# Kernel optimization log

Measured on AMD Instinct MI355X. Metric: run time of the kernel, lower is better.

The kernel has to match this reference:

```python
import jax, jax.numpy as jnp
import numpy as np

CELU_ALPHA = 3.0  # hardcoded in the torch module (nn.CELU(alpha=3.0), F.celu(alpha=3.0))

def celu(x):
    # celu(x, a) = max(0, x) + min(0, a*(exp(x/a)-1)); overflow-safe form
    return jnp.maximum(x, 0.0) + CELU_ALPHA * jnp.expm1(jnp.minimum(x, 0.0) / CELU_ALPHA)

def setup_inputs() -> dict:
    key = jax.random.key(0)
    k1, k2, k3, k4, k5 = jax.random.split(key, 5)
    N, E, H, D = 16384, 262144, 4, 64
    return {
        "features": jax.random.normal(k1, (N, D), dtype=jnp.float32),
        "metapath_embedding": jax.random.normal(k2, (E, D), dtype=jnp.float32),
        "attn1_w": jax.random.normal(k3, (H, D), dtype=jnp.float32) * 0.15,  # xavier-ish scale
        "attn2": jax.random.normal(k4, (H, D), dtype=jnp.float32) * 0.15,
        "segment_ids": jax.random.randint(k5, (E,), 0, N, dtype=jnp.int32),
    }

def reference(features, metapath_embedding, attn1_w, attn2, segment_ids):
    N, D = features.shape
    H = attn1_w.shape[0]
    # eft: same embedding broadcast over heads (torch.cat([emb]*H).view(-1,H,D))
    eft = celu(metapath_embedding)                    # [E, D]
    a1 = celu(features @ attn1_w.T)                   # [N, H] (per-node, shared across its instances)
    a2 = eft @ attn2.T                                # [E, H]
    a = celu(a1[segment_ids] + a2)                    # [E, H]
    # segment softmax over instances of each node
    m = jax.lax.stop_gradient(jax.ops.segment_max(a, segment_ids, num_segments=N))  # [N, H]
    ex = jnp.exp(a - m[segment_ids])                  # [E, H]
    denom = jax.ops.segment_sum(ex, segment_ids, num_segments=N)                    # [N, H]
    att = ex / denom[segment_ids]                     # [E, H]
    # weighted sum of eft over each node's instances -> [N, H, D]
    msg = jax.ops.segment_sum(att[:, :, None] * eft[:, None, :], segment_ids, num_segments=N)
    # empty segments yield 0 and celu(0)=0, matching the torch zero-fill branch
    return celu(msg).reshape(N, H * D)
```

## Files before the change

### kernel.cpp

```cpp
#include <hip/hip_runtime.h>
#include <math.h>

#define CAP 64

__device__ __forceinline__ float celu3(float x) {
    return fmaxf(x, 0.0f) + 3.0f * (__expf(fminf(x, 0.0f) * (1.0f / 3.0f)) - 1.0f);
}

__device__ __forceinline__ float wave_sum64(float v) {
#pragma unroll
    for (int off = 32; off > 0; off >>= 1) v += __shfl_xor(v, off, 64);
    return v;
}


__global__ __launch_bounds__(256) void zero_kernel(int* __restrict__ p, int n) {
    int i = blockIdx.x * 256 + threadIdx.x;
    if (i < n) p[i] = 0;
}


__global__ __launch_bounds__(256) void hist_a1_kernel(
    const int* __restrict__ seg, int* __restrict__ counts, int* __restrict__ elist, int E,
    const float* __restrict__ feat, const float* __restrict__ w1,
    float* __restrict__ a1, int N)
{
    int nblk_a1 = (N + 3) / 4;
    if ((int)blockIdx.x < nblk_a1) {
        int lane = threadIdx.x & 63;
        int wv = threadIdx.x >> 6;
        int n = blockIdx.x * 4 + wv;
        if (n >= N) return;
        float f = feat[(long)n * 64 + lane];
        float s[4];
#pragma unroll
        for (int h = 0; h < 4; ++h) s[h] = wave_sum64(f * w1[h * 64 + lane]);
        if (lane < 4) a1[n * 4 + lane] = celu3(s[lane]);
    } else {
        int i = (blockIdx.x - nblk_a1) * blockDim.x + threadIdx.x;
        int stride = 512 * blockDim.x;
        for (; i < E; i += stride) {
            int s = seg[i];
            int r = atomicAdd(&counts[s], 1);
            if (r < CAP) elist[s * CAP + r] = i;
        }
    }
}


__global__ __launch_bounds__(256) void fused_kernel(
    const float* __restrict__ meta, const float* __restrict__ w2,
    const float* __restrict__ a1, const int* __restrict__ counts,
    const int* __restrict__ elist, const int* __restrict__ seg,
    float* __restrict__ out, int N, int E)
{
    int t = threadIdx.x;
    int lane = t & 63;
    int wv = t >> 6;
    int n = blockIdx.x * 4 + wv;
    if (n >= N) return;

    int cnt = counts[n];
    int g = lane >> 4;
    int q = lane & 15;
    long ob = (long)n * 256 + g * 64 + q * 4;

    if (cnt == 0) {
        float4 z = {0.f, 0.f, 0.f, 0.f};
        *(float4*)(out + ob) = z;
        return;
    }

    float4 a1v = *(const float4*)(a1 + (long)n * 4);

    if (cnt <= CAP) {
        float4 w2q0 = *(const float4*)(w2 + 0 * 64 + q * 4);
        float4 w2q1 = *(const float4*)(w2 + 1 * 64 + q * 4);
        float4 w2q2 = *(const float4*)(w2 + 2 * 64 + q * 4);
        float4 w2q3 = *(const float4*)(w2 + 3 * 64 + q * 4);

        int eid_l = (lane < cnt) ? elist[n * CAP + lane] : 0;

        float sp0 = 0.f, sp1 = 0.f, sp2 = 0.f, sp3 = 0.f;
        float4 acc0 = {0,0,0,0}, acc1 = {0,0,0,0}, acc2 = {0,0,0,0}, acc3 = {0,0,0,0};

        int nch = (cnt + 3) >> 2;
#pragma unroll 4
        for (int c = 0; c < nch; ++c) {
            int j = c * 4 + g;
            bool vr = j < cnt;
            int eid = __shfl(eid_l, j);
            float4 v = *(const float4*)(meta + (long)eid * 64 + q * 4);
            float4 ef;
            ef.x = celu3(v.x); ef.y = celu3(v.y); ef.z = celu3(v.z); ef.w = celu3(v.w);

            float d0 = ef.x * w2q0.x + ef.y * w2q0.y + ef.z * w2q0.z + ef.w * w2q0.w;
            float d1 = ef.x * w2q1.x + ef.y * w2q1.y + ef.z * w2q1.z + ef.w * w2q1.w;
            float d2 = ef.x * w2q2.x + ef.y * w2q2.y + ef.z * w2q2.z + ef.w * w2q2.w;
            float d3 = ef.x * w2q3.x + ef.y * w2q3.y + ef.z * w2q3.z + ef.w * w2q3.w;
#pragma unroll
            for (int off = 1; off < 16; off <<= 1) {
                d0 += __shfl_xor(d0, off); d1 += __shfl_xor(d1, off);
                d2 += __shfl_xor(d2, off); d3 += __shfl_xor(d3, off);
            }

            float A0 = vr ? celu3(a1v.x + d0) : -INFINITY;
            float A1 = vr ? celu3(a1v.y + d1) : -INFINITY;
            float A2 = vr ? celu3(a1v.z + d2) : -INFINITY;
            float A3 = vr ? celu3(a1v.w + d3) : -INFINITY;

            float p0 = __expf(fminf(A0, 80.f));
            float p1 = __expf(fminf(A1, 80.f));
            float p2 = __expf(fminf(A2, 80.f));
            float p3 = __expf(fminf(A3, 80.f));

            sp0 += p0; sp1 += p1; sp2 += p2; sp3 += p3;

            acc0.x = fmaf(p0, ef.x, acc0.x); acc0.y = fmaf(p0, ef.y, acc0.y);
            acc0.z = fmaf(p0, ef.z, acc0.z); acc0.w = fmaf(p0, ef.w, acc0.w);
            acc1.x = fmaf(p1, ef.x, acc1.x); acc1.y = fmaf(p1, ef.y, acc1.y);
            acc1.z = fmaf(p1, ef.z, acc1.z); acc1.w = fmaf(p1, ef.w, acc1.w);
            acc2.x = fmaf(p2, ef.x, acc2.x); acc2.y = fmaf(p2, ef.y, acc2.y);
            acc2.z = fmaf(p2, ef.z, acc2.z); acc2.w = fmaf(p2, ef.w, acc2.w);
            acc3.x = fmaf(p3, ef.x, acc3.x); acc3.y = fmaf(p3, ef.y, acc3.y);
            acc3.z = fmaf(p3, ef.z, acc3.z); acc3.w = fmaf(p3, ef.w, acc3.w);
        }

        sp0 += __shfl_xor(sp0, 16); sp0 += __shfl_xor(sp0, 32);
        sp1 += __shfl_xor(sp1, 16); sp1 += __shfl_xor(sp1, 32);
        sp2 += __shfl_xor(sp2, 16); sp2 += __shfl_xor(sp2, 32);
        sp3 += __shfl_xor(sp3, 16); sp3 += __shfl_xor(sp3, 32);

        acc0.x += __shfl_xor(acc0.x, 16); acc0.x += __shfl_xor(acc0.x, 32);
        acc0.y += __shfl_xor(acc0.y, 16); acc0.y += __shfl_xor(acc0.y, 32);
        acc0.z += __shfl_xor(acc0.z, 16); acc0.z += __shfl_xor(acc0.z, 32);
        acc0.w += __shfl_xor(acc0.w, 16); acc0.w += __shfl_xor(acc0.w, 32);
        acc1.x += __shfl_xor(acc1.x, 16); acc1.x += __shfl_xor(acc1.x, 32);
        acc1.y += __shfl_xor(acc1.y, 16); acc1.y += __shfl_xor(acc1.y, 32);
        acc1.z += __shfl_xor(acc1.z, 16); acc1.z += __shfl_xor(acc1.z, 32);
        acc1.w += __shfl_xor(acc1.w, 16); acc1.w += __shfl_xor(acc1.w, 32);
        acc2.x += __shfl_xor(acc2.x, 16); acc2.x += __shfl_xor(acc2.x, 32);
        acc2.y += __shfl_xor(acc2.y, 16); acc2.y += __shfl_xor(acc2.y, 32);
        acc2.z += __shfl_xor(acc2.z, 16); acc2.z += __shfl_xor(acc2.z, 32);
        acc2.w += __shfl_xor(acc2.w, 16); acc2.w += __shfl_xor(acc2.w, 32);
        acc3.x += __shfl_xor(acc3.x, 16); acc3.x += __shfl_xor(acc3.x, 32);
        acc3.y += __shfl_xor(acc3.y, 16); acc3.y += __shfl_xor(acc3.y, 32);
        acc3.z += __shfl_xor(acc3.z, 16); acc3.z += __shfl_xor(acc3.z, 32);
        acc3.w += __shfl_xor(acc3.w, 16); acc3.w += __shfl_xor(acc3.w, 32);

        float rs0 = 1.f / sp0, rs1 = 1.f / sp1, rs2 = 1.f / sp2, rs3 = 1.f / sp3;

        float4 av = (g == 0) ? acc0 : (g == 1) ? acc1 : (g == 2) ? acc2 : acc3;
        float rg = (g == 0) ? rs0 : (g == 1) ? rs1 : (g == 2) ? rs2 : rs3;
        float4 o;
        o.x = celu3(av.x * rg); o.y = celu3(av.y * rg);
        o.z = celu3(av.z * rg); o.w = celu3(av.w * rg);
        *(float4*)(out + ob) = o;
        return;
    }

    {
        float a10 = a1v.x, a11 = a1v.y, a12 = a1v.z, a13 = a1v.w;
        float w2v0 = w2[0 * 64 + lane], w2v1 = w2[1 * 64 + lane];
        float w2v2 = w2[2 * 64 + lane], w2v3 = w2[3 * 64 + lane];
        float m0 = -INFINITY, m1 = -INFINITY, m2 = -INFINITY, m3 = -INFINITY;
        float s0 = 0.f, s1 = 0.f, s2 = 0.f, s3 = 0.f;
        float ac0 = 0.f, ac1 = 0.f, ac2 = 0.f, ac3 = 0.f;
        for (int base = 0; base < E; base += 64) {
            int e = base + lane;
            bool hit = (e < E) && (seg[e] == n);
            unsigned long long ball = __ballot(hit);
            while (ball) {
                int b = __ffsll((long long)ball) - 1;
                ball &= ball - 1;
                int eid = base + b;
                float eft = celu3(meta[(long)eid * 64 + lane]);
                float d0 = wave_sum64(eft * w2v0);
                float d1 = wave_sum64(eft * w2v1);
                float d2 = wave_sum64(eft * w2v2);
                float d3 = wave_sum64(eft * w2v3);
                float A0 = celu3(a10 + d0), A1 = celu3(a11 + d1);
                float A2 = celu3(a12 + d2), A3 = celu3(a13 + d3);
                float nm0 = fmaxf(m0, A0), nm1 = fmaxf(m1, A1);
                float nm2 = fmaxf(m2, A2), nm3 = fmaxf(m3, A3);
                float al0 = __expf(m0 - nm0), al1 = __expf(m1 - nm1);
                float al2 = __expf(m2 - nm2), al3 = __expf(m3 - nm3);
                float p0 = __expf(A0 - nm0), p1 = __expf(A1 - nm1);
                float p2 = __expf(A2 - nm2), p3 = __expf(A3 - nm3);
                s0 = fmaf(al0, s0, p0); s1 = fmaf(al1, s1, p1);
                s2 = fmaf(al2, s2, p2); s3 = fmaf(al3, s3, p3);
                ac0 = fmaf(p0, eft, al0 * ac0); ac1 = fmaf(p1, eft, al1 * ac1);
                ac2 = fmaf(p2, eft, al2 * ac2); ac3 = fmaf(p3, eft, al3 * ac3);
                m0 = nm0; m1 = nm1; m2 = nm2; m3 = nm3;
            }
        }
        long ob2 = (long)n * 256 + lane;
        out[ob2]       = celu3(ac0 / s0);
        out[ob2 + 64]  = celu3(ac1 / s1);
        out[ob2 + 128] = celu3(ac2 / s2);
        out[ob2 + 192] = celu3(ac3 / s3);
    }
}


extern "C" void kernel_launch(void* const* d_in, const int* in_sizes, int n_in,
                              void* d_out, int out_size, void* d_ws, size_t ws_size,
                              hipStream_t stream)
{
    const float* feat = (const float*)d_in[0];
    const float* meta = (const float*)d_in[1];
    const float* w1   = (const float*)d_in[2];
    const float* w2   = (const float*)d_in[3];
    const int*   seg  = (const int*)d_in[4];
    float* out = (float*)d_out;

    int N = in_sizes[0] / 64;
    int E = in_sizes[4];

    float* a1   = (float*)d_ws;
    int* counts = (int*)(a1 + (size_t)N * 4);
    int* elist  = counts + N;

    int nblk_a1 = (N + 3) / 4;

    zero_kernel<<<(N + 255) / 256, 256, 0, stream>>>(counts, N);
    hist_a1_kernel<<<nblk_a1 + 512, 256, 0, stream>>>(seg, counts, elist, E, feat, w1, a1, N);
    fused_kernel<<<(N + 3) / 4, 256, 0, stream>>>(meta, w2, a1, counts, elist, seg, out, N, E);
}
```

Measured before the change: 55.17 us.

## Precompute per-edge attention dot products in a separate pass before node aggregation

Moves the per-edge celu(meta)·attn2 dot product out of the per-node gather loop into a streaming pass, one thread per edge. That pass runs in the same launch as the histogram atomics and writes a float4 per edge to workspace. The node kernel then computes softmax weights once per edge in-lane and broadcasts them with shuffles, dropping the 16-lane shuffle reductions. The zeroing kernel is folded into the a1 kernel to save a launch. The trade-off is a second full read of the metapath embeddings plus extra workspace traffic for the dot products.

Measured after the change: 58.39 us. 1.06x slower.

```diff
diff --git a/kernel.cpp b/kernel.cpp
--- a/kernel.cpp
+++ b/kernel.cpp
@@ -14,45 +14,71 @@
 }
 
 
-__global__ __launch_bounds__(256) void zero_kernel(int* __restrict__ p, int n) {
-    int i = blockIdx.x * 256 + threadIdx.x;
-    if (i < n) p[i] = 0;
-}
-
-
-__global__ __launch_bounds__(256) void hist_a1_kernel(
+__global__ __launch_bounds__(256) void init_kernel(
+    int* __restrict__ counts, int N,
+    const float* __restrict__ feat, const float* __restrict__ w1,
+    float* __restrict__ a1)
+{
+    int nblk_zero = (N + 255) / 256;
+    if ((int)blockIdx.x < nblk_zero) {
+        int i = blockIdx.x * 256 + threadIdx.x;
+        if (i < N) counts[i] = 0;
+        return;
+    }
+    int n = (blockIdx.x - nblk_zero) * 4 + (threadIdx.x >> 6);
+    int lane = threadIdx.x & 63;
+    if (n >= N) return;
+    float f = feat[(long)n * 64 + lane];
+    float s[4];
+#pragma unroll
+    for (int h = 0; h < 4; ++h) s[h] = wave_sum64(f * w1[h * 64 + lane]);
+    if (lane < 4) a1[n * 4 + lane] = celu3(s[lane]);
+}
+
+
+__global__ __launch_bounds__(256) void hist_dot_kernel(
     const int* __restrict__ seg, int* __restrict__ counts, int* __restrict__ elist, int E,
-    const float* __restrict__ feat, const float* __restrict__ w1,
-    float* __restrict__ a1, int N)
-{
-    int nblk_a1 = (N + 3) / 4;
-    if ((int)blockIdx.x < nblk_a1) {
-        int lane = threadIdx.x & 63;
-        int wv = threadIdx.x >> 6;
-        int n = blockIdx.x * 4 + wv;
-        if (n >= N) return;
-        float f = feat[(long)n * 64 + lane];
-        float s[4];
-#pragma unroll
-        for (int h = 0; h < 4; ++h) s[h] = wave_sum64(f * w1[h * 64 + lane]);
-        if (lane < 4) a1[n * 4 + lane] = celu3(s[lane]);
-    } else {
-        int i = (blockIdx.x - nblk_a1) * blockDim.x + threadIdx.x;
-        int stride = 512 * blockDim.x;
+    const float* __restrict__ meta, const float* __restrict__ w2,
+    float4* __restrict__ d4)
+{
+    if ((int)blockIdx.x < 512) {
+        int i = blockIdx.x * 256 + threadIdx.x;
+        int stride = 512 * 256;
         for (; i < E; i += stride) {
             int s = seg[i];
             int r = atomicAdd(&counts[s], 1);
             if (r < CAP) elist[s * CAP + r] = i;
         }
-    }
-}
-
-
-__global__ __launch_bounds__(256) void fused_kernel(
+        return;
+    }
+    int e = (blockIdx.x - 512) * 256 + threadIdx.x;
+    if (e >= E) return;
+    const float4* row = (const float4*)(meta + (long)e * 64);
+    float d0 = 0.f, d1 = 0.f, d2 = 0.f, d3 = 0.f;
+#pragma unroll
+    for (int k = 0; k < 16; ++k) {
+        float4 v = row[k];
+        float4 ef;
+        ef.x = celu3(v.x); ef.y = celu3(v.y); ef.z = celu3(v.z); ef.w = celu3(v.w);
+        float4 w0 = *(const float4*)(w2 + 0 * 64 + k * 4);
+        float4 w1v = *(const float4*)(w2 + 1 * 64 + k * 4);
+        float4 w2v = *(const float4*)(w2 + 2 * 64 + k * 4);
+        float4 w3v = *(const float4*)(w2 + 3 * 64 + k * 4);
+        d0 += ef.x * w0.x + ef.y * w0.y + ef.z * w0.z + ef.w * w0.w;
+        d1 += ef.x * w1v.x + ef.y * w1v.y + ef.z * w1v.z + ef.w * w1v.w;
+        d2 += ef.x * w2v.x + ef.y * w2v.y + ef.z * w2v.z + ef.w * w2v.w;
+        d3 += ef.x * w3v.x + ef.y * w3v.y + ef.z * w3v.z + ef.w * w3v.w;
+    }
+    float4 o; o.x = d0; o.y = d1; o.z = d2; o.w = d3;
+    d4[e] = o;
+}
+
+
+__global__ __launch_bounds__(256) void node_kernel(
     const float* __restrict__ meta, const float* __restrict__ w2,
     const float* __restrict__ a1, const int* __restrict__ counts,
-    const int* __restrict__ elist, const int* __restrict__ seg,
-    float* __restrict__ out, int N, int E)
+    const int* __restrict__ elist, const float4* __restrict__ d4,
+    const int* __restrict__ seg, float* __restrict__ out, int N, int E)
 {
     int t = threadIdx.x;
     int lane = t & 63;
@@ -74,56 +100,44 @@
     float4 a1v = *(const float4*)(a1 + (long)n * 4);
 
     if (cnt <= CAP) {
-        float4 w2q0 = *(const float4*)(w2 + 0 * 64 + q * 4);
-        float4 w2q1 = *(const float4*)(w2 + 1 * 64 + q * 4);
-        float4 w2q2 = *(const float4*)(w2 + 2 * 64 + q * 4);
-        float4 w2q3 = *(const float4*)(w2 + 3 * 64 + q * 4);
-
-        int eid_l = (lane < cnt) ? elist[n * CAP + lane] : 0;
+        bool valid = lane < cnt;
+        int eid_l = valid ? elist[n * CAP + lane] : 0;
+        float p0 = 0.f, p1 = 0.f, p2 = 0.f, p3 = 0.f;
+        if (valid) {
+            float4 dv = d4[eid_l];
+            float A0 = celu3(a1v.x + dv.x);
+            float A1 = celu3(a1v.y + dv.y);
+            float A2 = celu3(a1v.z + dv.z);
+            float A3 = celu3(a1v.w + dv.w);
+            p0 = __expf(fminf(A0, 80.f));
+            p1 = __expf(fminf(A1, 80.f));
+            p2 = __expf(fminf(A2, 80.f));
+            p3 = __expf(fminf(A3, 80.f));
+        }
 
         float sp0 = 0.f, sp1 = 0.f, sp2 = 0.f, sp3 = 0.f;
         float4 acc0 = {0,0,0,0}, acc1 = {0,0,0,0}, acc2 = {0,0,0,0}, acc3 = {0,0,0,0};
-
         int nch = (cnt + 3) >> 2;
 #pragma unroll 4
         for (int c = 0; c < nch; ++c) {
             int j = c * 4 + g;
-            bool vr = j < cnt;
             int eid = __shfl(eid_l, j);
+            float b0 = __shfl(p0, j);
+            float b1 = __shfl(p1, j);
+            float b2 = __shfl(p2, j);
+            float b3 = __shfl(p3, j);
+            sp0 += b0; sp1 += b1; sp2 += b2; sp3 += b3;
             float4 v = *(const float4*)(meta + (long)eid * 64 + q * 4);
             float4 ef;
             ef.x = celu3(v.x); ef.y = celu3(v.y); ef.z = celu3(v.z); ef.w = celu3(v.w);
-
-            float d0 = ef.x * w2q0.x + ef.y * w2q0.y + ef.z * w2q0.z + ef.w * w2q0.w;
-            float d1 = ef.x * w2q1.x + ef.y * w2q1.y + ef.z * w2q1.z + ef.w * w2q1.w;
-            float d2 = ef.x * w2q2.x + ef.y * w2q2.y + ef.z * w2q2.z + ef.w * w2q2.w;
-            float d3 = ef.x * w2q3.x + ef.y * w2q3.y + ef.z * w2q3.z + ef.w * w2q3.w;
-#pragma unroll
-            for (int off = 1; off < 16; off <<= 1) {
-                d0 += __shfl_xor(d0, off); d1 += __shfl_xor(d1, off);
-                d2 += __shfl_xor(d2, off); d3 += __shfl_xor(d3, off);
-            }
-
-            float A0 = vr ? celu3(a1v.x + d0) : -INFINITY;
-            float A1 = vr ? celu3(a1v.y + d1) : -INFINITY;
-            float A2 = vr ? celu3(a1v.z + d2) : -INFINITY;
-            float A3 = vr ? celu3(a1v.w + d3) : -INFINITY;
-
-            float p0 = __expf(fminf(A0, 80.f));
-            float p1 = __expf(fminf(A1, 80.f));
-            float p2 = __expf(fminf(A2, 80.f));
-            float p3 = __expf(fminf(A3, 80.f));
-
-            sp0 += p0; sp1 += p1; sp2 += p2; sp3 += p3;
-
-            acc0.x = fmaf(p0, ef.x, acc0.x); acc0.y = fmaf(p0, ef.y, acc0.y);
-            acc0.z = fmaf(p0, ef.z, acc0.z); acc0.w = fmaf(p0, ef.w, acc0.w);
-            acc1.x = fmaf(p1, ef.x, acc1.x); acc1.y = fmaf(p1, ef.y, acc1.y);
-            acc1.z = fmaf(p1, ef.z, acc1.z); acc1.w = fmaf(p1, ef.w, acc1.w);
-            acc2.x = fmaf(p2, ef.x, acc2.x); acc2.y = fmaf(p2, ef.y, acc2.y);
-            acc2.z = fmaf(p2, ef.z, acc2.z); acc2.w = fmaf(p2, ef.w, acc2.w);
-            acc3.x = fmaf(p3, ef.x, acc3.x); acc3.y = fmaf(p3, ef.y, acc3.y);
-            acc3.z = fmaf(p3, ef.z, acc3.z); acc3.w = fmaf(p3, ef.w, acc3.w);
+            acc0.x = fmaf(b0, ef.x, acc0.x); acc0.y = fmaf(b0, ef.y, acc0.y);
+            acc0.z = fmaf(b0, ef.z, acc0.z); acc0.w = fmaf(b0, ef.w, acc0.w);
+            acc1.x = fmaf(b1, ef.x, acc1.x); acc1.y = fmaf(b1, ef.y, acc1.y);
+            acc1.z = fmaf(b1, ef.z, acc1.z); acc1.w = fmaf(b1, ef.w, acc1.w);
+            acc2.x = fmaf(b2, ef.x, acc2.x); acc2.y = fmaf(b2, ef.y, acc2.y);
+            acc2.z = fmaf(b2, ef.z, acc2.z); acc2.w = fmaf(b2, ef.w, acc2.w);
+            acc3.x = fmaf(b3, ef.x, acc3.x); acc3.y = fmaf(b3, ef.y, acc3.y);
+            acc3.z = fmaf(b3, ef.z, acc3.z); acc3.w = fmaf(b3, ef.w, acc3.w);
         }
 
         sp0 += __shfl_xor(sp0, 16); sp0 += __shfl_xor(sp0, 32);
@@ -217,13 +231,16 @@
     int N = in_sizes[0] / 64;
     int E = in_sizes[4];
 
-    float* a1   = (float*)d_ws;
-    int* counts = (int*)(a1 + (size_t)N * 4);
-    int* elist  = counts + N;
-
-    int nblk_a1 = (N + 3) / 4;
-
-    zero_kernel<<<(N + 255) / 256, 256, 0, stream>>>(counts, N);
-    hist_a1_kernel<<<nblk_a1 + 512, 256, 0, stream>>>(seg, counts, elist, E, feat, w1, a1, N);
-    fused_kernel<<<(N + 3) / 4, 256, 0, stream>>>(meta, w2, a1, counts, elist, seg, out, N, E);
-}
+    float4* d4   = (float4*)d_ws;
+    float*  a1   = (float*)(d4 + E);
+    int* counts  = (int*)(a1 + (size_t)N * 4);
+    int* elist   = counts + N;
+
+    int nblk_zero = (N + 255) / 256;
+    int nblk_a1   = (N + 3) / 4;
+    int nblk_dot  = (E + 255) / 256;
+
+    init_kernel<<<nblk_zero + nblk_a1, 256, 0, stream>>>(counts, N, feat, w1, a1);
+    hist_dot_kernel<<<512 + nblk_dot, 256, 0, stream>>>(seg, counts, elist, E, meta, w2, d4);
+    node_kernel<<<(N + 3) / 4, 256, 0, stream>>>(meta, w2, a1, counts, elist, d4, seg, out, N, E);
+}
```
